# Kernel optimization log

Measured on AMD Instinct MI355X. Metric: run time of the kernel, lower is better.

Reference implementation:

```python
import jax, jax.numpy as jnp
import numpy as np

B, Lq, Skv = 4, 512, 4096
INPUT_DIM, QUERY_DIM, HIDDEN_DIM, CROSS_HEAD = 256, 256, 512, 8
MID_DIM = HIDDEN_DIM // 2          # 256, V/output width
HEAD_DIM = QUERY_DIM // CROSS_HEAD # 32
VHEAD_DIM = MID_DIM // CROSS_HEAD  # 32


def setup_inputs() -> dict:
    key = jax.random.key(0)
    ks = jax.random.split(key, 8)
    query = jax.random.normal(ks[0], (B, Lq, INPUT_DIM), dtype=jnp.float32)
    key_value = jax.random.normal(ks[1], (B, Skv, INPUT_DIM), dtype=jnp.float32)
    mask = jax.random.randint(ks[2], (B, Skv), 0, 2, dtype=jnp.int32)
    s = 1.0 / np.sqrt(INPUT_DIM)
    Wq = jax.random.normal(ks[3], (INPUT_DIM, QUERY_DIM), dtype=jnp.float32) * s
    Wk = jax.random.normal(ks[4], (INPUT_DIM, QUERY_DIM), dtype=jnp.float32) * s
    Wv = jax.random.normal(ks[5], (INPUT_DIM, MID_DIM), dtype=jnp.float32) * s
    Wo = jax.random.normal(ks[6], (MID_DIM, HIDDEN_DIM), dtype=jnp.float32) * (1.0 / np.sqrt(MID_DIM))
    bo = jax.random.normal(ks[7], (HIDDEN_DIM,), dtype=jnp.float32) * 0.01
    return {"query": query, "key_value": key_value, "mask": mask,
            "Wq": Wq, "Wk": Wk, "Wv": Wv, "Wo": Wo, "bo": bo}


def reference(query, key_value, mask, Wq, Wk, Wv, Wo, bo):
    scale = jnp.asarray(np.sqrt(HEAD_DIM), dtype=query.dtype)
    # Projections
    Q = (query @ Wq).reshape(B, Lq, CROSS_HEAD, HEAD_DIM).transpose(0, 2, 1, 3)      # [B,H,Lq,dh]
    K = (key_value @ Wk).reshape(B, Skv, CROSS_HEAD, HEAD_DIM).transpose(0, 2, 1, 3)  # [B,H,Skv,dh]
    V = (key_value @ Wv).reshape(B, Skv, CROSS_HEAD, VHEAD_DIM).transpose(0, 2, 1, 3) # [B,H,Skv,dv]
    # Scaled dot-product energy
    energy = jnp.einsum('bhqd,bhkd->bhqk', Q, K) / scale                              # [B,H,Lq,Skv]
    # Key-padding mask broadcast over heads and query positions
    keep = (mask[:, None, None, :] != 0)                                              # [B,1,1,Skv]
    energy = jnp.where(keep, energy, -jnp.inf)
    attention = jax.nn.softmax(energy, axis=-1)
    # dropout_ratio = 0 -> identity
    x = jnp.einsum('bhqk,bhkd->bhqd', attention, V)                                   # [B,H,Lq,dv]
    x = x.transpose(0, 2, 1, 3).reshape(B, Lq, MID_DIM)
    x = x @ Wo + bo                                                                   # [B,Lq,HIDDEN_DIM]
    return (x, attention, energy)
```

## Files before the change

kernel.cpp:

```cpp
#include <hip/hip_runtime.h>
#include <cstdint>
#include <cmath>

#define INV_SCALE 0.17677669529663687f
#define NEG_BIG   (-1e30f)

__device__ __forceinline__ void unpack8(float* d, float4 a, float4 b) {
  d[0]=a.x; d[1]=a.y; d[2]=a.z; d[3]=a.w; d[4]=b.x; d[5]=b.y; d[6]=b.z; d[7]=b.w;
}

__device__ __forceinline__ void gemm_64x128(const float* __restrict__ A,
                                            const float* __restrict__ W,
                                            float* __restrict__ C,
                                            int m0, int n0, int N) {
  __shared__ float At[16][68];
  __shared__ float Ws[16][132];
  const int t   = threadIdx.x;
  const int mg  = t & 15;
  const int ng  = t >> 4;
  const int am  = t & 63;
  const int ak4 = (t >> 6) << 2;
  const int wk  = t >> 4;
  const int wn8 = (t & 15) << 3;

  float acc[4][8];
#pragma unroll
  for (int i = 0; i < 4; ++i)
#pragma unroll
    for (int j = 0; j < 8; ++j) acc[i][j] = 0.f;

  float4 a0 = *(const float4*)&A[(size_t)(m0 + am) * 256 + ak4];
  float4 w0 = *(const float4*)&W[(size_t)wk * N + n0 + wn8];
  float4 w1 = *(const float4*)&W[(size_t)wk * N + n0 + wn8 + 4];

  for (int k0 = 0; k0 < 256; k0 += 16) {
    __syncthreads();
    At[ak4 + 0][am] = a0.x; At[ak4 + 1][am] = a0.y;
    At[ak4 + 2][am] = a0.z; At[ak4 + 3][am] = a0.w;
    *(float4*)&Ws[wk][wn8]     = w0;
    *(float4*)&Ws[wk][wn8 + 4] = w1;
    __syncthreads();
    if (k0 + 16 < 256) {
      a0 = *(const float4*)&A[(size_t)(m0 + am) * 256 + k0 + 16 + ak4];
      w0 = *(const float4*)&W[(size_t)(k0 + 16 + wk) * N + n0 + wn8];
      w1 = *(const float4*)&W[(size_t)(k0 + 16 + wk) * N + n0 + wn8 + 4];
    }
#pragma unroll 4
    for (int kk = 0; kk < 16; ++kk) {
      float av[4], wv[8];
      *(float4*)av = *(const float4*)&At[kk][mg * 4];
      unpack8(wv, *(const float4*)&Ws[kk][ng * 8], *(const float4*)&Ws[kk][ng * 8 + 4]);
#pragma unroll
      for (int i = 0; i < 4; ++i)
#pragma unroll
        for (int j = 0; j < 8; ++j) acc[i][j] += av[i] * wv[j];
    }
  }

#pragma unroll
  for (int i = 0; i < 4; ++i) {
    float4 o0, o1;
    o0.x = acc[i][0]; o0.y = acc[i][1]; o0.z = acc[i][2]; o0.w = acc[i][3];
    o1.x = acc[i][4]; o1.y = acc[i][5]; o1.z = acc[i][6]; o1.w = acc[i][7];
    float* dst = &C[(size_t)(m0 + mg * 4 + i) * N + n0 + ng * 8];
    *(float4*)dst       = o0;
    *(float4*)(dst + 4) = o1;
  }
}

__global__ __launch_bounds__(256) void proj3_kernel(
    const float* __restrict__ q_in, const float* __restrict__ kv_in,
    const float* __restrict__ Wq, const float* __restrict__ Wk,
    const float* __restrict__ Wv, float* __restrict__ Qp,
    float* __restrict__ Kp, float* __restrict__ Vp) {
  const float* A; const float* W; float* C; int M;
  if (blockIdx.z == 0)      { A = q_in;  W = Wq; C = Qp; M = 2048;  }
  else if (blockIdx.z == 1) { A = kv_in; W = Wk; C = Kp; M = 16384; }
  else                      { A = kv_in; W = Wv; C = Vp; M = 16384; }
  int m0 = blockIdx.x * 64;
  if (m0 >= M) return;
  gemm_64x128(A, W, C, m0, blockIdx.y * 128, 256);
}

__global__ __launch_bounds__(256) void out_proj_kernel(
    const float* __restrict__ xmid, const float* __restrict__ Wo,
    const float* __restrict__ bo, float* __restrict__ out) {
  __shared__ float At[16][68];
  __shared__ float Ws[16][68];
  const int t   = threadIdx.x;
  const int mg  = t & 15;
  const int ng  = t >> 4;
  const int am  = t & 63;
  const int ak4 = (t >> 6) << 2;
  const int wk  = t >> 4;
  const int wn4 = (t & 15) << 2;
  const int m0 = blockIdx.x * 64, n0 = blockIdx.y * 64;

  float acc[4][4];
#pragma unroll
  for (int i = 0; i < 4; ++i)
#pragma unroll
    for (int j = 0; j < 4; ++j) acc[i][j] = 0.f;

  float4 a0 = *(const float4*)&xmid[(size_t)(m0 + am) * 256 + ak4];
  float4 w0 = *(const float4*)&Wo[(size_t)wk * 512 + n0 + wn4];

  for (int k0 = 0; k0 < 256; k0 += 16) {
    __syncthreads();
    At[ak4 + 0][am] = a0.x; At[ak4 + 1][am] = a0.y;
    At[ak4 + 2][am] = a0.z; At[ak4 + 3][am] = a0.w;
    *(float4*)&Ws[wk][wn4] = w0;
    __syncthreads();
    if (k0 + 16 < 256) {
      a0 = *(const float4*)&xmid[(size_t)(m0 + am) * 256 + k0 + 16 + ak4];
      w0 = *(const float4*)&Wo[(size_t)(k0 + 16 + wk) * 512 + n0 + wn4];
    }
#pragma unroll 4
    for (int kk = 0; kk < 16; ++kk) {
      float av[4], wv[4];
      *(float4*)av = *(const float4*)&At[kk][mg * 4];
      *(float4*)wv = *(const float4*)&Ws[kk][ng * 4];
#pragma unroll
      for (int i = 0; i < 4; ++i)
#pragma unroll
        for (int j = 0; j < 4; ++j) acc[i][j] += av[i] * wv[j];
    }
  }

#pragma unroll
  for (int i = 0; i < 4; ++i) {
    float4 o;
    o.x = acc[i][0] + bo[n0 + ng * 4 + 0];
    o.y = acc[i][1] + bo[n0 + ng * 4 + 1];
    o.z = acc[i][2] + bo[n0 + ng * 4 + 2];
    o.w = acc[i][3] + bo[n0 + ng * 4 + 3];
    *(float4*)&out[(size_t)(m0 + mg * 4 + i) * 512 + n0 + ng * 4] = o;
  }
}

__global__ __launch_bounds__(256) void energy_kernel(
    const float* __restrict__ Qp, const float* __restrict__ Kp,
    const int* __restrict__ mask, float* __restrict__ Eout,
    float* __restrict__ pm, float* __restrict__ ps) {
  __shared__ float Qt[32][68];
  __shared__ float Kt[32][260];
  __shared__ float redM[32][65];
  __shared__ float redS[32][65];
  __shared__ float redM2[4][65];
  __shared__ float redS2[4][65];
  __shared__ int   msk[256];
  const int t  = threadIdx.x;
  const int bh = blockIdx.y, b = bh >> 3, h = bh & 7;
  const int q0 = blockIdx.x * 64;
  const int kbase = blockIdx.z * 1024;
  const int mg = t & 7;
  const int kg = t >> 3;

  {
    int m = t >> 2, i8 = (t & 3) << 3;
    const float* src = &Qp[(size_t)(b * 512 + q0 + m) * 256 + h * 32 + i8];
    float4 v0 = *(const float4*)src;
    float4 v1 = *(const float4*)(src + 4);
    Qt[i8 + 0][m] = v0.x; Qt[i8 + 1][m] = v0.y; Qt[i8 + 2][m] = v0.z; Qt[i8 + 3][m] = v0.w;
    Qt[i8 + 4][m] = v1.x; Qt[i8 + 5][m] = v1.y; Qt[i8 + 6][m] = v1.z; Qt[i8 + 7][m] = v1.w;
  }

  float m_run = NEG_BIG, s_run = 0.f;

  float kr[32];
  {
    const float* src = &Kp[(size_t)(b * 4096 + kbase + t) * 256 + h * 32];
#pragma unroll
    for (int u = 0; u < 8; ++u) *(float4*)&kr[u * 4] = *(const float4*)(src + u * 4);
  }
  int mv = mask[b * 4096 + kbase + t];

  for (int kc = 0; kc < 1024; kc += 256) {
    __syncthreads();
#pragma unroll
    for (int i = 0; i < 32; ++i) Kt[i][t] = kr[i];
    msk[t] = mv;
    __syncthreads();
    if (kc + 256 < 1024) {
      const float* src = &Kp[(size_t)(b * 4096 + kbase + kc + 256 + t) * 256 + h * 32];
#pragma unroll
      for (int u = 0; u < 8; ++u) *(float4*)&kr[u * 4] = *(const float4*)(src + u * 4);
      mv = mask[b * 4096 + kbase + kc + 256 + t];
    }

    float e[8][8];
#pragma unroll
    for (int i = 0; i < 8; ++i)
#pragma unroll
      for (int j = 0; j < 8; ++j) e[i][j] = 0.f;

#pragma unroll 4
    for (int i = 0; i < 32; ++i) {
      float qa[8], ka[8];
      unpack8(qa, *(const float4*)&Qt[i][mg * 8], *(const float4*)&Qt[i][mg * 8 + 4]);
      unpack8(ka, *(const float4*)&Kt[i][kg * 8], *(const float4*)&Kt[i][kg * 8 + 4]);
#pragma unroll
      for (int qi = 0; qi < 8; ++qi)
#pragma unroll
        for (int kj = 0; kj < 8; ++kj) e[qi][kj] += qa[qi] * ka[kj];
    }

    int km[8];
#pragma unroll
    for (int j = 0; j < 8; ++j) km[j] = msk[kg * 8 + j];

#pragma unroll
    for (int iq = 0; iq < 8; ++iq) {
      int q = mg * 8 + iq;
      float v[8];
#pragma unroll
      for (int j = 0; j < 8; ++j) {
        float ev = e[iq][j] * INV_SCALE;
        v[j] = (km[j] != 0) ? ev : NEG_BIG;
      }
      size_t base = ((size_t)(bh * 512 + q0 + q)) * 4096 + kbase + kc + kg * 8;
      *(float4*)&Eout[base]     = make_float4(v[0], v[1], v[2], v[3]);
      *(float4*)&Eout[base + 4] = make_float4(v[4], v[5], v[6], v[7]);
      float mx = fmaxf(fmaxf(fmaxf(v[0], v[1]), fmaxf(v[2], v[3])),
                       fmaxf(fmaxf(v[4], v[5]), fmaxf(v[6], v[7])));
      float ss = __expf(v[0] - mx) + __expf(v[1] - mx) + __expf(v[2] - mx) + __expf(v[3] - mx)
               + __expf(v[4] - mx) + __expf(v[5] - mx) + __expf(v[6] - mx) + __expf(v[7] - mx);
      redM[kg][q] = mx;
      redS[kg][q] = ss;
    }
    __syncthreads();
    {
      int r = t & 63, sub = t >> 6;
      float M = NEG_BIG;
#pragma unroll
      for (int g = sub * 8; g < sub * 8 + 8; ++g) M = fmaxf(M, redM[g][r]);
      float S = 0.f;
#pragma unroll
      for (int g = sub * 8; g < sub * 8 + 8; ++g) S += redS[g][r] * __expf(redM[g][r] - M);
      redM2[sub][r] = M;
      redS2[sub][r] = S;
    }
    __syncthreads();
    if (t < 64) {
      float M = NEG_BIG;
#pragma unroll
      for (int s = 0; s < 4; ++s) M = fmaxf(M, redM2[s][t]);
      float S = 0.f;
#pragma unroll
      for (int s = 0; s < 4; ++s) S += redS2[s][t] * __expf(redM2[s][t] - M);
      float nm = fmaxf(m_run, M);
      s_run = s_run * __expf(m_run - nm) + S * __expf(M - nm);
      m_run = nm;
    }
  }
  if (t < 64) {
    pm[(size_t)blockIdx.z * 16384 + bh * 512 + q0 + t] = m_run;
    ps[(size_t)blockIdx.z * 16384 + bh * 512 + q0 + t] = s_run;
  }
}

__global__ __launch_bounds__(256) void merge_stats_kernel(
    const float* __restrict__ pm, const float* __restrict__ ps,
    float* __restrict__ mrow, float* __restrict__ rrow) {
  int r = blockIdx.x * 256 + threadIdx.x;
  float m0 = pm[r], m1 = pm[16384 + r], m2 = pm[32768 + r], m3 = pm[49152 + r];
  float M = fmaxf(fmaxf(m0, m1), fmaxf(m2, m3));
  float S = ps[r]         * __expf(m0 - M) + ps[16384 + r] * __expf(m1 - M)
          + ps[32768 + r] * __expf(m2 - M) + ps[49152 + r] * __expf(m3 - M);
  mrow[r] = M;
  rrow[r] = 1.0f / S;
}

__global__ __launch_bounds__(256) void attn_pv_kernel(
    const float* __restrict__ Ein, const float* __restrict__ Vp,
    const float* __restrict__ mrow, const float* __restrict__ rrow,
    float* __restrict__ Aout, float* __restrict__ xmid) {
  __shared__ float At4[4][32][36];
  __shared__ float Vs[128][36];
  __shared__ float mq[32], rq[32];
  __shared__ float pvred[32 * 33];
  const int t  = threadIdx.x;
  const int bh = blockIdx.y, b = bh >> 3, h = bh & 7;
  const int q0 = blockIdx.x * 32;
  const int qg = t & 3;
  const int dg = (t >> 2) & 3;
  const int ks = t >> 4;
  const int vk = t >> 1, vi = (t & 1) << 4;
  const int aq = t >> 5, an = t & 31;

  if (t < 32) {
    mq[t] = mrow[bh * 512 + q0 + t];
    rq[t] = rrow[bh * 512 + q0 + t];
  }

  float acc[8][8];
#pragma unroll
  for (int i = 0; i < 8; ++i)
#pragma unroll
    for (int j = 0; j < 8; ++j) acc[i][j] = 0.f;

  float4 vr0, vr1, vr2, vr3;
  {
    const float* src = &Vp[(size_t)(b * 4096 + vk) * 256 + h * 32 + vi];
    vr0 = *(const float4*)(src);     vr1 = *(const float4*)(src + 4);
    vr2 = *(const float4*)(src + 8); vr3 = *(const float4*)(src + 12);
  }
  float4 evp[4];
#pragma unroll
  for (int p = 0; p < 4; ++p)
    evp[p] = *(const float4*)&Ein[((size_t)(bh * 512 + q0 + aq + p * 8)) * 4096 + an * 4];

  __syncthreads();

  for (int kc = 0; kc < 4096; kc += 128) {
    *(float4*)&Vs[vk][vi]      = vr0;
    *(float4*)&Vs[vk][vi + 4]  = vr1;
    *(float4*)&Vs[vk][vi + 8]  = vr2;
    *(float4*)&Vs[vk][vi + 12] = vr3;
#pragma unroll
    for (int p = 0; p < 4; ++p) {
      int q = aq + p * 8;
      size_t base = ((size_t)(bh * 512 + q0 + q)) * 4096 + kc + an * 4;
      float4 ev = evp[p];
      float m = mq[q], r = rq[q];
      float4 av;
      av.x = __expf(ev.x - m) * r;
      av.y = __expf(ev.y - m) * r;
      av.z = __expf(ev.z - m) * r;
      av.w = __expf(ev.w - m) * r;
      *(float4*)&Aout[base] = av;
      At4[0][an][q] = av.x;
      At4[1][an][q] = av.y;
      At4[2][an][q] = av.z;
      At4[3][an][q] = av.w;
    }
    __syncthreads();
    if (kc + 128 < 4096) {
      const float* src = &Vp[(size_t)(b * 4096 + kc + 128 + vk) * 256 + h * 32 + vi];
      vr0 = *(const float4*)(src);     vr1 = *(const float4*)(src + 4);
      vr2 = *(const float4*)(src + 8); vr3 = *(const float4*)(src + 12);
#pragma unroll
      for (int p = 0; p < 4; ++p)
        evp[p] = *(const float4*)&Ein[((size_t)(bh * 512 + q0 + aq + p * 8)) * 4096
                                      + kc + 128 + an * 4];
    }
#pragma unroll 4
    for (int kk = 0; kk < 8; ++kk) {
      int k  = ks * 8 + kk;
      int m_ = k >> 2;
      int j_ = k & 3;
      float a[8], v[8];
      unpack8(a, *(const float4*)&At4[j_][m_][qg * 8], *(const float4*)&At4[j_][m_][qg * 8 + 4]);
      unpack8(v, *(const float4*)&Vs[k][dg * 8],       *(const float4*)&Vs[k][dg * 8 + 4]);
#pragma unroll
      for (int i = 0; i < 8; ++i)
#pragma unroll
        for (int j = 0; j < 8; ++j) acc[i][j] += a[i] * v[j];
    }
    __syncthreads();
  }

  for (int s = 0; s < 16; ++s) {
    if (ks == s) {
#pragma unroll
      for (int i = 0; i < 8; ++i)
#pragma unroll
        for (int j = 0; j < 8; ++j) {
          int q = qg * 8 + i, d = dg * 8 + j;
          if (s == 0) pvred[q * 33 + d] = acc[i][j];
          else        pvred[q * 33 + d] += acc[i][j];
        }
    }
    __syncthreads();
  }
  for (int idx = t; idx < 1024; idx += 256) {
    int q = idx >> 5, d = idx & 31;
    xmid[((size_t)(b * 512) + q0 + q) * 256 + h * 32 + d] = pvred[q * 33 + d];
  }
}

extern "C" void kernel_launch(void* const* d_in, const int* in_sizes, int n_in,
                              void* d_out, int out_size, void* d_ws, size_t ws_size,
                              hipStream_t stream) {
  const float* query     = (const float*)d_in[0];
  const float* key_value = (const float*)d_in[1];
  const int*   mask      = (const int*)  d_in[2];
  const float* Wq        = (const float*)d_in[3];
  const float* Wk        = (const float*)d_in[4];
  const float* Wv        = (const float*)d_in[5];
  const float* Wo        = (const float*)d_in[6];
  const float* bo        = (const float*)d_in[7];

  float* out        = (float*)d_out;
  float* x_out      = out;
  float* attn_out   = out + 1048576;
  float* energy_out = out + 68157440;

  float* ws   = (float*)d_ws;
  float* Qp   = ws;
  float* Kp   = ws + 524288;
  float* Vp   = ws + 4718592;
  float* xmid = ws + 8912896;
  float* pm   = xmid;
  float* ps   = xmid + 65536;
  float* mrow = ws + 9437184;
  float* rrow = ws + 9453568;

  proj3_kernel<<<dim3(256, 2, 3), 256, 0, stream>>>(query, key_value, Wq, Wk, Wv,
                                                    Qp, Kp, Vp);
  energy_kernel<<<dim3(8, 32, 4), 256, 0, stream>>>(Qp, Kp, mask, energy_out, pm, ps);
  merge_stats_kernel<<<dim3(64), 256, 0, stream>>>(pm, ps, mrow, rrow);
  attn_pv_kernel<<<dim3(16, 32), 256, 0, stream>>>(energy_out, Vp, mrow, rrow,
                                                   attn_out, xmid);
  out_proj_kernel<<<dim3(32, 8), 256, 0, stream>>>(xmid, Wo, bo, x_out);
}
```

Baseline: 788.3 us.

## Split PV over key halves, shrink energy tile, coalesce global tile loads

The attention-PV kernel now splits the key dimension into two halves across blockIdx.z, which doubles the grid. Each half writes a partial xmid: one into the old xmid slot and one into the now-dead Qp buffer. The output projection sums the two partials as it loads A. The energy kernel uses 128-key chunks with a 4x8 per-thread tile instead of 256 keys with 8x8, cutting shared memory and registers so more blocks fit per CU. Global loads of A, K and V are remapped so that adjacent threads read contiguous row segments. The costs are an extra partial-sum read in out_proj, more LDS transpose stores, and reuse of Qp as scratch.

```diff
diff --git a/kernel.cpp b/kernel.cpp
--- a/kernel.cpp
+++ b/kernel.cpp
@@ -18,8 +18,8 @@
   const int t   = threadIdx.x;
   const int mg  = t & 15;
   const int ng  = t >> 4;
-  const int am  = t & 63;
-  const int ak4 = (t >> 6) << 2;
+  const int ar  = t >> 2;
+  const int ac  = (t & 3) << 2;
   const int wk  = t >> 4;
   const int wn8 = (t & 15) << 3;
 
@@ -29,19 +29,19 @@
 #pragma unroll
     for (int j = 0; j < 8; ++j) acc[i][j] = 0.f;
 
-  float4 a0 = *(const float4*)&A[(size_t)(m0 + am) * 256 + ak4];
+  float4 a0 = *(const float4*)&A[(size_t)(m0 + ar) * 256 + ac];
   float4 w0 = *(const float4*)&W[(size_t)wk * N + n0 + wn8];
   float4 w1 = *(const float4*)&W[(size_t)wk * N + n0 + wn8 + 4];
 
   for (int k0 = 0; k0 < 256; k0 += 16) {
     __syncthreads();
-    At[ak4 + 0][am] = a0.x; At[ak4 + 1][am] = a0.y;
-    At[ak4 + 2][am] = a0.z; At[ak4 + 3][am] = a0.w;
+    At[ac + 0][ar] = a0.x; At[ac + 1][ar] = a0.y;
+    At[ac + 2][ar] = a0.z; At[ac + 3][ar] = a0.w;
     *(float4*)&Ws[wk][wn8]     = w0;
     *(float4*)&Ws[wk][wn8 + 4] = w1;
     __syncthreads();
     if (k0 + 16 < 256) {
-      a0 = *(const float4*)&A[(size_t)(m0 + am) * 256 + k0 + 16 + ak4];
+      a0 = *(const float4*)&A[(size_t)(m0 + ar) * 256 + k0 + 16 + ac];
       w0 = *(const float4*)&W[(size_t)(k0 + 16 + wk) * N + n0 + wn8];
       w1 = *(const float4*)&W[(size_t)(k0 + 16 + wk) * N + n0 + wn8 + 4];
     }
@@ -83,15 +83,16 @@
 }
 
 __global__ __launch_bounds__(256) void out_proj_kernel(
-    const float* __restrict__ xmid, const float* __restrict__ Wo,
-    const float* __restrict__ bo, float* __restrict__ out) {
+    const float* __restrict__ x0, const float* __restrict__ x1,
+    const float* __restrict__ Wo, const float* __restrict__ bo,
+    float* __restrict__ out) {
   __shared__ float At[16][68];
   __shared__ float Ws[16][68];
   const int t   = threadIdx.x;
   const int mg  = t & 15;
   const int ng  = t >> 4;
-  const int am  = t & 63;
-  const int ak4 = (t >> 6) << 2;
+  const int ar  = t >> 2;
+  const int ac  = (t & 3) << 2;
   const int wk  = t >> 4;
   const int wn4 = (t & 15) << 2;
   const int m0 = blockIdx.x * 64, n0 = blockIdx.y * 64;
@@ -102,17 +103,19 @@
 #pragma unroll
     for (int j = 0; j < 4; ++j) acc[i][j] = 0.f;
 
-  float4 a0 = *(const float4*)&xmid[(size_t)(m0 + am) * 256 + ak4];
+  float4 a0 = *(const float4*)&x0[(size_t)(m0 + ar) * 256 + ac];
+  float4 a1 = *(const float4*)&x1[(size_t)(m0 + ar) * 256 + ac];
   float4 w0 = *(const float4*)&Wo[(size_t)wk * 512 + n0 + wn4];
 
   for (int k0 = 0; k0 < 256; k0 += 16) {
     __syncthreads();
-    At[ak4 + 0][am] = a0.x; At[ak4 + 1][am] = a0.y;
-    At[ak4 + 2][am] = a0.z; At[ak4 + 3][am] = a0.w;
+    At[ac + 0][ar] = a0.x + a1.x; At[ac + 1][ar] = a0.y + a1.y;
+    At[ac + 2][ar] = a0.z + a1.z; At[ac + 3][ar] = a0.w + a1.w;
     *(float4*)&Ws[wk][wn4] = w0;
     __syncthreads();
     if (k0 + 16 < 256) {
-      a0 = *(const float4*)&xmid[(size_t)(m0 + am) * 256 + k0 + 16 + ak4];
+      a0 = *(const float4*)&x0[(size_t)(m0 + ar) * 256 + k0 + 16 + ac];
+      a1 = *(const float4*)&x1[(size_t)(m0 + ar) * 256 + k0 + 16 + ac];
       w0 = *(const float4*)&Wo[(size_t)(k0 + 16 + wk) * 512 + n0 + wn4];
     }
 #pragma unroll 4
@@ -143,18 +146,20 @@
     const int* __restrict__ mask, float* __restrict__ Eout,
     float* __restrict__ pm, float* __restrict__ ps) {
   __shared__ float Qt[32][68];
-  __shared__ float Kt[32][260];
-  __shared__ float redM[32][65];
-  __shared__ float redS[32][65];
-  __shared__ float redM2[4][65];
-  __shared__ float redS2[4][65];
-  __shared__ int   msk[256];
+  __shared__ float Kt[32][132];
+  __shared__ float redM[16][65];
+  __shared__ float redS[16][65];
+  __shared__ float red2M[4][65];
+  __shared__ float red2S[4][65];
+  __shared__ int   msk[128];
   const int t  = threadIdx.x;
   const int bh = blockIdx.y, b = bh >> 3, h = bh & 7;
   const int q0 = blockIdx.x * 64;
   const int kbase = blockIdx.z * 1024;
-  const int mg = t & 7;
-  const int kg = t >> 3;
+  const int mg = t & 15;
+  const int kg = t >> 4;
+  const int krr = t >> 3;
+  const int krc = (t & 7) << 2;
 
   {
     int m = t >> 2, i8 = (t & 3) << 3;
@@ -167,40 +172,45 @@
 
   float m_run = NEG_BIG, s_run = 0.f;
 
-  float kr[32];
-  {
-    const float* src = &Kp[(size_t)(b * 4096 + kbase + t) * 256 + h * 32];
-#pragma unroll
-    for (int u = 0; u < 8; ++u) *(float4*)&kr[u * 4] = *(const float4*)(src + u * 4);
-  }
-  int mv = mask[b * 4096 + kbase + t];
-
-  for (int kc = 0; kc < 1024; kc += 256) {
-    __syncthreads();
-#pragma unroll
-    for (int i = 0; i < 32; ++i) Kt[i][t] = kr[i];
-    msk[t] = mv;
-    __syncthreads();
-    if (kc + 256 < 1024) {
-      const float* src = &Kp[(size_t)(b * 4096 + kbase + kc + 256 + t) * 256 + h * 32];
-#pragma unroll
-      for (int u = 0; u < 8; ++u) *(float4*)&kr[u * 4] = *(const float4*)(src + u * 4);
-      mv = mask[b * 4096 + kbase + kc + 256 + t];
-    }
-
-    float e[8][8];
-#pragma unroll
-    for (int i = 0; i < 8; ++i)
+  float4 kr4[4];
+#pragma unroll
+  for (int j = 0; j < 4; ++j)
+    kr4[j] = *(const float4*)&Kp[(size_t)(b * 4096 + kbase + krr + 32 * j) * 256 + h * 32 + krc];
+  int mv = (t < 128) ? mask[b * 4096 + kbase + t] : 0;
+
+  for (int kc = 0; kc < 1024; kc += 128) {
+    __syncthreads();
+#pragma unroll
+    for (int j = 0; j < 4; ++j) {
+      int kr = krr + 32 * j;
+      Kt[krc + 0][kr] = kr4[j].x;
+      Kt[krc + 1][kr] = kr4[j].y;
+      Kt[krc + 2][kr] = kr4[j].z;
+      Kt[krc + 3][kr] = kr4[j].w;
+    }
+    if (t < 128) msk[t] = mv;
+    __syncthreads();
+    if (kc + 128 < 1024) {
+#pragma unroll
+      for (int j = 0; j < 4; ++j)
+        kr4[j] = *(const float4*)&Kp[(size_t)(b * 4096 + kbase + kc + 128 + krr + 32 * j) * 256
+                                     + h * 32 + krc];
+      if (t < 128) mv = mask[b * 4096 + kbase + kc + 128 + t];
+    }
+
+    float e[4][8];
+#pragma unroll
+    for (int i = 0; i < 4; ++i)
 #pragma unroll
       for (int j = 0; j < 8; ++j) e[i][j] = 0.f;
 
 #pragma unroll 4
     for (int i = 0; i < 32; ++i) {
-      float qa[8], ka[8];
-      unpack8(qa, *(const float4*)&Qt[i][mg * 8], *(const float4*)&Qt[i][mg * 8 + 4]);
+      float qa[4], ka[8];
+      *(float4*)qa = *(const float4*)&Qt[i][mg * 4];
       unpack8(ka, *(const float4*)&Kt[i][kg * 8], *(const float4*)&Kt[i][kg * 8 + 4]);
 #pragma unroll
-      for (int qi = 0; qi < 8; ++qi)
+      for (int qi = 0; qi < 4; ++qi)
 #pragma unroll
         for (int kj = 0; kj < 8; ++kj) e[qi][kj] += qa[qi] * ka[kj];
     }
@@ -210,8 +220,8 @@
     for (int j = 0; j < 8; ++j) km[j] = msk[kg * 8 + j];
 
 #pragma unroll
-    for (int iq = 0; iq < 8; ++iq) {
-      int q = mg * 8 + iq;
+    for (int iq = 0; iq < 4; ++iq) {
+      int q = mg * 4 + iq;
       float v[8];
 #pragma unroll
       for (int j = 0; j < 8; ++j) {
@@ -233,21 +243,21 @@
       int r = t & 63, sub = t >> 6;
       float M = NEG_BIG;
 #pragma unroll
-      for (int g = sub * 8; g < sub * 8 + 8; ++g) M = fmaxf(M, redM[g][r]);
+      for (int g = sub * 4; g < sub * 4 + 4; ++g) M = fmaxf(M, redM[g][r]);
       float S = 0.f;
 #pragma unroll
-      for (int g = sub * 8; g < sub * 8 + 8; ++g) S += redS[g][r] * __expf(redM[g][r] - M);
-      redM2[sub][r] = M;
-      redS2[sub][r] = S;
+      for (int g = sub * 4; g < sub * 4 + 4; ++g) S += redS[g][r] * __expf(redM[g][r] - M);
+      red2M[sub][r] = M;
+      red2S[sub][r] = S;
     }
     __syncthreads();
     if (t < 64) {
       float M = NEG_BIG;
 #pragma unroll
-      for (int s = 0; s < 4; ++s) M = fmaxf(M, redM2[s][t]);
+      for (int s = 0; s < 4; ++s) M = fmaxf(M, red2M[s][t]);
       float S = 0.f;
 #pragma unroll
-      for (int s = 0; s < 4; ++s) S += redS2[s][t] * __expf(redM2[s][t] - M);
+      for (int s = 0; s < 4; ++s) S += red2S[s][t] * __expf(red2M[s][t] - M);
       float nm = fmaxf(m_run, M);
       s_run = s_run * __expf(m_run - nm) + S * __expf(M - nm);
       m_run = nm;
@@ -274,18 +284,20 @@
 __global__ __launch_bounds__(256) void attn_pv_kernel(
     const float* __restrict__ Ein, const float* __restrict__ Vp,
     const float* __restrict__ mrow, const float* __restrict__ rrow,
-    float* __restrict__ Aout, float* __restrict__ xmid) {
+    float* __restrict__ Aout, float* __restrict__ xmid0,
+    float* __restrict__ xmid1) {
   __shared__ float At4[4][32][36];
   __shared__ float Vs[128][36];
   __shared__ float mq[32], rq[32];
-  __shared__ float pvred[32 * 33];
   const int t  = threadIdx.x;
   const int bh = blockIdx.y, b = bh >> 3, h = bh & 7;
   const int q0 = blockIdx.x * 32;
+  const int kbase = blockIdx.z * 2048;
   const int qg = t & 3;
   const int dg = (t >> 2) & 3;
   const int ks = t >> 4;
-  const int vk = t >> 1, vi = (t & 1) << 4;
+  const int vrr = t >> 3;
+  const int vrc = (t & 7) << 2;
   const int aq = t >> 5, an = t & 31;
 
   if (t < 32) {
@@ -299,28 +311,26 @@
 #pragma unroll
     for (int j = 0; j < 8; ++j) acc[i][j] = 0.f;
 
-  float4 vr0, vr1, vr2, vr3;
-  {
-    const float* src = &Vp[(size_t)(b * 4096 + vk) * 256 + h * 32 + vi];
-    vr0 = *(const float4*)(src);     vr1 = *(const float4*)(src + 4);
-    vr2 = *(const float4*)(src + 8); vr3 = *(const float4*)(src + 12);
-  }
+  float4 vr4[4];
+#pragma unroll
+  for (int j = 0; j < 4; ++j)
+    vr4[j] = *(const float4*)&Vp[(size_t)(b * 4096 + kbase + vrr + 32 * j) * 256 + h * 32 + vrc];
   float4 evp[4];
 #pragma unroll
   for (int p = 0; p < 4; ++p)
-    evp[p] = *(const float4*)&Ein[((size_t)(bh * 512 + q0 + aq + p * 8)) * 4096 + an * 4];
+    evp[p] = *(const float4*)&Ein[((size_t)(bh * 512 + q0 + aq + p * 8)) * 4096
+                                  + kbase + an * 4];
 
   __syncthreads();
 
-  for (int kc = 0; kc < 4096; kc += 128) {
-    *(float4*)&Vs[vk][vi]      = vr0;
-    *(float4*)&Vs[vk][vi + 4]  = vr1;
-    *(float4*)&Vs[vk][vi + 8]  = vr2;
-    *(float4*)&Vs[vk][vi + 12] = vr3;
+  for (int kc = 0; kc < 2048; kc += 128) {
+#pragma unroll
+    for (int j = 0; j < 4; ++j)
+      *(float4*)&Vs[vrr + 32 * j][vrc] = vr4[j];
 #pragma unroll
     for (int p = 0; p < 4; ++p) {
       int q = aq + p * 8;
-      size_t base = ((size_t)(bh * 512 + q0 + q)) * 4096 + kc + an * 4;
+      size_t base = ((size_t)(bh * 512 + q0 + q)) * 4096 + kbase + kc + an * 4;
       float4 ev = evp[p];
       float m = mq[q], r = rq[q];
       float4 av;
@@ -335,14 +345,15 @@
       At4[3][an][q] = av.w;
     }
     __syncthreads();
-    if (kc + 128 < 4096) {
-      const float* src = &Vp[(size_t)(b * 4096 + kc + 128 + vk) * 256 + h * 32 + vi];
-      vr0 = *(const float4*)(src);     vr1 = *(const float4*)(src + 4);
-      vr2 = *(const float4*)(src + 8); vr3 = *(const float4*)(src + 12);
+    if (kc + 128 < 2048) {
+#pragma unroll
+      for (int j = 0; j < 4; ++j)
+        vr4[j] = *(const float4*)&Vp[(size_t)(b * 4096 + kbase + kc + 128 + vrr + 32 * j) * 256
+                                     + h * 32 + vrc];
 #pragma unroll
       for (int p = 0; p < 4; ++p)
         evp[p] = *(const float4*)&Ein[((size_t)(bh * 512 + q0 + aq + p * 8)) * 4096
-                                      + kc + 128 + an * 4];
+                                      + kbase + kc + 128 + an * 4];
     }
 #pragma unroll 4
     for (int kk = 0; kk < 8; ++kk) {
@@ -360,6 +371,7 @@
     __syncthreads();
   }
 
+  float* pvred = &At4[0][0][0];
   for (int s = 0; s < 16; ++s) {
     if (ks == s) {
 #pragma unroll
@@ -373,9 +385,10 @@
     }
     __syncthreads();
   }
+  float* part = (blockIdx.z == 0) ? xmid0 : xmid1;
   for (int idx = t; idx < 1024; idx += 256) {
     int q = idx >> 5, d = idx & 31;
-    xmid[((size_t)(b * 512) + q0 + q) * 256 + h * 32 + d] = pvred[q * 33 + d];
+    part[((size_t)(b * 512) + q0 + q) * 256 + h * 32 + d] = pvred[q * 33 + d];
   }
 }
 
@@ -396,21 +409,22 @@
   float* attn_out   = out + 1048576;
   float* energy_out = out + 68157440;
 
-  float* ws   = (float*)d_ws;
-  float* Qp   = ws;
-  float* Kp   = ws + 524288;
-  float* Vp   = ws + 4718592;
-  float* xmid = ws + 8912896;
-  float* pm   = xmid;
-  float* ps   = xmid + 65536;
-  float* mrow = ws + 9437184;
-  float* rrow = ws + 9453568;
+  float* ws    = (float*)d_ws;
+  float* Qp    = ws;
+  float* Kp    = ws + 524288;
+  float* Vp    = ws + 4718592;
+  float* xmid0 = ws + 8912896;
+  float* xmid1 = Qp;
+  float* pm    = xmid0;
+  float* ps    = xmid0 + 65536;
+  float* mrow  = ws + 9437184;
+  float* rrow  = ws + 9453568;
 
   proj3_kernel<<<dim3(256, 2, 3), 256, 0, stream>>>(query, key_value, Wq, Wk, Wv,
                                                     Qp, Kp, Vp);
   energy_kernel<<<dim3(8, 32, 4), 256, 0, stream>>>(Qp, Kp, mask, energy_out, pm, ps);
   merge_stats_kernel<<<dim3(64), 256, 0, stream>>>(pm, ps, mrow, rrow);
-  attn_pv_kernel<<<dim3(16, 32), 256, 0, stream>>>(energy_out, Vp, mrow, rrow,
-                                                   attn_out, xmid);
-  out_proj_kernel<<<dim3(32, 8), 256, 0, stream>>>(xmid, Wo, bo, x_out);
-}
+  attn_pv_kernel<<<dim3(16, 32, 2), 256, 0, stream>>>(energy_out, Vp, mrow, rrow,
+                                                      attn_out, xmid0, xmid1);
+  out_proj_kernel<<<dim3(32, 8), 256, 0, stream>>>(xmid0, xmid1, Wo, bo, x_out);
+}
```

Result: slower. 827.9 us (+5.0%).
